# Kernel tuning notes

Hardware: AMD Instinct MI355X
Metric: run time of the kernel (lower is better)

The kernel has to match this reference:

```python
import math
import jax, jax.numpy as jnp
import numpy as np

# hyperparameters matching init_kwargs / spoco defaults
DELTA_VAR = 0.5
DELTA_DIST = 2.0
ALPHA = 1.0
BETA = 1.0
GAMMA = 0.001
INSTANCE_W = 1.0
PMAPS_THRESHOLD = 0.9  # gaussian-kernel threshold: pmap==PMAPS_THRESHOLD at dist==delta_var
EPS = 1e-6


def setup_inputs() -> dict:
    key = jax.random.key(0)
    k1, k2 = jax.random.split(key)
    N, E, H, W, C = 4, 64, 512, 512, 64
    embeddings = jax.random.normal(k1, (N, E, H, W), dtype=jnp.float32)
    target = jax.random.randint(k2, (N, H, W), 0, C)
    return {"embeddings": embeddings, "target": target, "n_instances": C}


def _single_item_loss(emb, tgt, C):
    """emb: (E,H,W) float, tgt: (H,W) int labels in [0,C). Returns scalar loss."""
    E = emb.shape[0]
    P = emb.shape[1] * emb.shape[2]
    e = emb.reshape(E, P)            # (E,P)
    t = tgt.reshape(P)               # (P,)

    # --- cluster means via segment reduce (math-equivalent to one-hot expand+sum) ---
    counts = jax.ops.segment_sum(jnp.ones((P,), e.dtype), t, num_segments=C)  # (C,)
    sums = jax.ops.segment_sum(e.T, t, num_segments=C)                         # (C,E)
    safe_counts = jnp.maximum(counts, 1.0)
    means = sums / safe_counts[:, None]                                        # (C,E)

    # --- variance (pull) term ---
    mean_at_pix = means[t]                                                     # (P,E)
    dist = jnp.sqrt(jnp.sum((e.T - mean_at_pix) ** 2, axis=1) + 1e-12)         # (P,)
    hinged = jnp.maximum(dist - DELTA_VAR, 0.0) ** 2                           # hinge_pull=True
    var_term = jnp.sum(hinged / safe_counts[t]) / C

    # --- distance (push) term between cluster means ---
    diff = means[:, None, :] - means[None, :, :]                               # (C,C,E)
    dmat = jnp.sqrt(jnp.sum(diff ** 2, axis=-1) + 1e-12)                       # (C,C)
    repulsion = 2.0 * DELTA_DIST * (1.0 - jnp.eye(C, dtype=e.dtype))
    hinged_d = jnp.maximum(repulsion - dmat, 0.0) ** 2
    dist_term = jnp.sum(hinged_d) / (C * (C - 1))

    # --- regularization term ---
    reg_term = jnp.sum(jnp.sqrt(jnp.sum(means ** 2, axis=1) + 1e-12)) / C

    # --- instance term: differentiable gaussian instance pmaps vs one-hot masks (dice) ---
    two_sigma = DELTA_VAR ** 2 / (-math.log(PMAPS_THRESHOLD))
    # squared distance of every pixel embedding to every cluster mean, (C,P)
    d2 = (jnp.sum(e ** 2, axis=0)[None, :]
          + jnp.sum(means ** 2, axis=1)[:, None]
          - 2.0 * means @ e)
    d2 = jnp.maximum(d2, 0.0)
    pmaps = jnp.exp(-d2 / two_sigma)                                           # (C,P)
    masks = (t[None, :] == jnp.arange(C)[:, None]).astype(e.dtype)             # (C,P)
    intersect = jnp.sum(pmaps * masks, axis=1)
    denom = jnp.sum(pmaps ** 2, axis=1) + jnp.sum(masks, axis=1)
    dice = 2.0 * intersect / jnp.maximum(denom, EPS)                            # (C,)
    instance_term = 1.0 - jnp.mean(dice)

    return (ALPHA * var_term + BETA * dist_term + GAMMA * reg_term
            + INSTANCE_W * instance_term)


def reference(embeddings, target, n_instances):
    per_item = jax.vmap(lambda e, t: _single_item_loss(e, t, n_instances))(embeddings, target)
    return jnp.mean(per_item)
```

## Files before the change

kernel.cpp:

```cpp
#include <hip/hip_runtime.h>
#include <math.h>

#define NIT 4
#define ED  64
#define CL  64
#define PX  262144

#define W_CNT 0
#define W_SUM 256
#define W_MSQ 16640
#define W_INT 16896
#define W_DEN 17152
#define W_VAR 17408
#define W_DR  17412
#define W_TOT 17416

__device__ __forceinline__ void atomAddG(float* p, float v){
  __hip_atomic_fetch_add(p, v, __ATOMIC_RELAXED, __HIP_MEMORY_SCOPE_AGENT);
}
__device__ __forceinline__ void atomAddL(float* p, float v){
  __hip_atomic_fetch_add(p, v, __ATOMIC_RELAXED, __HIP_MEMORY_SCOPE_WORKGROUP);
}

__global__ __launch_bounds__(256) void k_sums(const float* __restrict__ emb,
                                              const int* __restrict__ tgt,
                                              float* __restrict__ ws){
  __shared__ float s_sum[CL*65];
  __shared__ float s_cnt[CL];
  const int tid = threadIdx.x;
  for (int i = tid; i < CL*65; i += 256) s_sum[i] = 0.f;
  if (tid < CL) s_cnt[tid] = 0.f;
  __syncthreads();
  const int n   = blockIdx.x >> 7;
  const int blk = blockIdx.x & 127;
  const float* eb = emb + (size_t)n * ED * PX;
  const int*   tg = tgt + (size_t)n * PX;
  const int base = blk * 2048;
  const int4 t0 = *(const int4*)(tg + base + tid*4);
  const int4 t1 = *(const int4*)(tg + base + 1024 + tid*4);
  atomAddL(&s_cnt[t0.x], 1.f); atomAddL(&s_cnt[t0.y], 1.f);
  atomAddL(&s_cnt[t0.z], 1.f); atomAddL(&s_cnt[t0.w], 1.f);
  atomAddL(&s_cnt[t1.x], 1.f); atomAddL(&s_cnt[t1.y], 1.f);
  atomAddL(&s_cnt[t1.z], 1.f); atomAddL(&s_cnt[t1.w], 1.f);
  const int a0 = t0.x*65, a1 = t0.y*65, a2 = t0.z*65, a3 = t0.w*65;
  const int b0 = t1.x*65, b1 = t1.y*65, b2 = t1.z*65, b3 = t1.w*65;
  #pragma unroll 4
  for (int e = 0; e < ED; ++e){
    const float* row = eb + (size_t)e * PX + base;
    const float4 v0 = *(const float4*)(row + tid*4);
    const float4 v1 = *(const float4*)(row + 1024 + tid*4);
    atomAddL(&s_sum[a0+e], v0.x); atomAddL(&s_sum[a1+e], v0.y);
    atomAddL(&s_sum[a2+e], v0.z); atomAddL(&s_sum[a3+e], v0.w);
    atomAddL(&s_sum[b0+e], v1.x); atomAddL(&s_sum[b1+e], v1.y);
    atomAddL(&s_sum[b2+e], v1.z); atomAddL(&s_sum[b3+e], v1.w);
  }
  __syncthreads();
  float* wsum = ws + W_SUM + n*CL*ED;
  for (int i = tid; i < CL*ED; i += 256)
    atomAddG(&wsum[i], s_sum[(i>>6)*65 + (i&63)]);
  if (tid < CL) atomAddG(&ws[W_CNT + n*CL + tid], s_cnt[tid]);
}

__global__ __launch_bounds__(256) void k_fin(float* __restrict__ ws){
  __shared__ float sm[CL][ED+1];
  __shared__ float red[256];
  const int tid = threadIdx.x;
  const int n = blockIdx.x;
  float* wsum = ws + W_SUM + n*CL*ED;
  const float* wcnt = ws + W_CNT + n*CL;
  for (int i = tid; i < CL*ED; i += 256){
    const int c = i >> 6, e = i & 63;
    const float m = wsum[i] / fmaxf(wcnt[c], 1.f);
    sm[c][e] = m;
    wsum[i] = m;
  }
  __syncthreads();
  float reg_local = 0.f;
  if (tid < CL){
    float s = 0.f;
    #pragma unroll
    for (int e = 0; e < ED; ++e) s += sm[tid][e]*sm[tid][e];
    ws[W_MSQ + n*CL + tid] = s;
    reg_local = sqrtf(s + 1e-12f);
  }
  float pair_local = 0.f;
  for (int idx = tid; idx < CL*CL; idx += 256){
    const int i = idx >> 6, j = idx & 63;
    if (i != j){
      float s = 0.f;
      #pragma unroll
      for (int e = 0; e < ED; ++e){ const float d = sm[i][e]-sm[j][e]; s += d*d; }
      const float h = fmaxf(4.0f - sqrtf(s + 1e-12f), 0.f);
      pair_local += h*h;
    }
  }
  red[tid] = pair_local; __syncthreads();
  for (int s = 128; s > 0; s >>= 1){ if (tid < s) red[tid] += red[tid+s]; __syncthreads(); }
  const float pair_sum = red[0];
  __syncthreads();
  red[tid] = reg_local; __syncthreads();
  for (int s = 128; s > 0; s >>= 1){ if (tid < s) red[tid] += red[tid+s]; __syncthreads(); }
  if (tid == 0)
    ws[W_DR + n] = pair_sum / 4032.0f + 0.001f * red[0] / 64.0f;
}

__global__ __launch_bounds__(256) void k_main(const float* __restrict__ emb,
                                              const int* __restrict__ tgt,
                                              float* __restrict__ ws){
  __shared__ float s_m[CL*ED];
  __shared__ float s_msq[CL];
  __shared__ float s_icnt[CL];
  __shared__ float s_den[CL];
  __shared__ float s_int[CL];
  __shared__ float s_var[4];
  const int tid = threadIdx.x;
  const int n   = blockIdx.x >> 8;
  const int blk = blockIdx.x & 255;
  const float* wm = ws + W_SUM + n*CL*ED;
  for (int i = tid; i < CL*ED; i += 256) s_m[i] = wm[i];
  if (tid < CL){
    s_msq[tid] = ws[W_MSQ + n*CL + tid];
    s_icnt[tid] = 1.f / fmaxf(ws[W_CNT + n*CL + tid], 1.f);
    s_den[tid] = 0.f;
    s_int[tid] = 0.f;
  }
  __syncthreads();
  const float* eb = emb + (size_t)n * ED * PX;
  const int*   tg = tgt + (size_t)n * PX;
  const int lane = tid & 63;
  const float kExpScale = -0.42144206f;
  float var_local = 0.f;
  float den_mine = 0.f;
  for (int it = 0; it < 2; ++it){
    const int p0 = blk*1024 + it*512 + tid;
    const int p1 = p0 + 256;
    const int ta = tg[p0], tb = tg[p1];
    float ev0[ED], ev1[ED];
    float e2a = 0.f, e2b = 0.f;
    #pragma unroll
    for (int e = 0; e < ED; ++e){
      const float va = eb[(size_t)e*PX + p0];
      const float vb = eb[(size_t)e*PX + p1];
      ev0[e] = va; ev1[e] = vb;
      e2a += va*va; e2b += vb*vb;
    }
    float pmta = 0.f, pmtb = 0.f, d2ta = 0.f, d2tb = 0.f;
    #pragma unroll 2
    for (int c = 0; c < CL; ++c){
      const float4* mrow = (const float4*)&s_m[c*ED];
      float a0=0.f,a1=0.f,a2=0.f,a3=0.f, b0=0.f,b1=0.f,b2=0.f,b3=0.f;
      #pragma unroll
      for (int e4 = 0; e4 < ED/4; ++e4){
        const float4 m = mrow[e4];
        a0 += m.x*ev0[e4*4+0]; a1 += m.y*ev0[e4*4+1];
        a2 += m.z*ev0[e4*4+2]; a3 += m.w*ev0[e4*4+3];
        b0 += m.x*ev1[e4*4+0]; b1 += m.y*ev1[e4*4+1];
        b2 += m.z*ev1[e4*4+2]; b3 += m.w*ev1[e4*4+3];
      }
      const float dota = (a0+a1)+(a2+a3);
      const float dotb = (b0+b1)+(b2+b3);
      const float msq = s_msq[c];
      const float d2a = fmaxf(e2a + msq - 2.f*dota, 0.f);
      const float d2b = fmaxf(e2b + msq - 2.f*dotb, 0.f);
      const float pma = __expf(d2a * kExpScale);
      const float pmb = __expf(d2b * kExpScale);
      float r = pma*pma + pmb*pmb;
      #pragma unroll
      for (int m_ = 1; m_ < 64; m_ <<= 1) r += __shfl_xor(r, m_, 64);
      den_mine += (lane == c) ? r : 0.f;
      const bool oa = (c == ta), ob = (c == tb);
      pmta = oa ? pma : pmta; d2ta = oa ? d2a : d2ta;
      pmtb = ob ? pmb : pmtb; d2tb = ob ? d2b : d2tb;
    }
    atomAddL(&s_int[ta], pmta);
    atomAddL(&s_int[tb], pmtb);
    const float da = sqrtf(d2ta + 1e-12f), db = sqrtf(d2tb + 1e-12f);
    const float ha = fmaxf(da - 0.5f, 0.f), hb = fmaxf(db - 0.5f, 0.f);
    var_local += ha*ha*s_icnt[ta] + hb*hb*s_icnt[tb];
  }
  atomAddL(&s_den[lane], den_mine);
  #pragma unroll
  for (int m_ = 1; m_ < 64; m_ <<= 1) var_local += __shfl_xor(var_local, m_, 64);
  if (lane == 0) s_var[tid >> 6] = var_local;
  __syncthreads();
  if (tid < CL){
    atomAddG(&ws[W_DEN + n*CL + tid], s_den[tid]);
    atomAddG(&ws[W_INT + n*CL + tid], s_int[tid]);
  }
  if (tid == 0)
    atomAddG(&ws[W_VAR + n], s_var[0]+s_var[1]+s_var[2]+s_var[3]);
}

__global__ __launch_bounds__(256) void k_out(const float* __restrict__ ws,
                                             float* __restrict__ out){
  __shared__ float dsum[NIT];
  __shared__ float tot;
  const int tid = threadIdx.x;
  if (tid < NIT) dsum[tid] = 0.f;
  if (tid == 0) tot = 0.f;
  __syncthreads();
  const int n = tid >> 6, c = tid & 63;
  const float cnt   = ws[W_CNT + n*CL + c];
  const float inter = ws[W_INT + n*CL + c];
  const float den   = ws[W_DEN + n*CL + c] + cnt;
  const float dice  = 2.f * inter / fmaxf(den, 1e-6f);
  atomAddL(&dsum[n], dice);
  __syncthreads();
  if (tid < NIT){
    const float loss = ws[W_VAR + tid] / 64.0f
                     + ws[W_DR + tid]
                     + (1.f - dsum[tid] / 64.0f);
    atomAddL(&tot, loss);
  }
  __syncthreads();
  if (tid == 0) out[0] = tot * 0.25f;
}

extern "C" void kernel_launch(void* const* d_in, const int* in_sizes, int n_in,
                              void* d_out, int out_size, void* d_ws, size_t ws_size,
                              hipStream_t stream){
  (void)in_sizes; (void)n_in; (void)out_size; (void)ws_size;
  const float* emb = (const float*)d_in[0];
  const int*   tgt = (const int*)d_in[1];
  float* ws  = (float*)d_ws;
  float* out = (float*)d_out;
  hipMemsetAsync(d_ws, 0, W_TOT*sizeof(float), stream);
  k_sums<<<NIT*128, 256, 0, stream>>>(emb, tgt, ws);
  k_fin <<<NIT,     256, 0, stream>>>(ws);
  k_main<<<NIT*256, 256, 0, stream>>>(emb, tgt, ws);
  k_out <<<1,       256, 0, stream>>>(ws, out);
}
```

Baseline: 855.9 us.

## Remap sums and main kernels to lane-per-cluster with LDS-staged pixel tiles

Both the segment-sum and the main distance kernels now assign one cluster per lane and keep that cluster's mean or partial sum in registers. Each wave stages a tile of 32 pixels × 64 embedding dims into LDS and broadcasts each pixel to every lane. In the sums kernel this replaces per-element LDS atomics with masked FMAs. In the main kernel it replaces the per-cluster 64-lane shuffle reductions and the shared atomics with per-lane accumulators. The cost is heavy register pressure (64-float arrays) and redundant masked FMA work across all 64 lanes.

```diff
diff --git a/kernel.cpp b/kernel.cpp
--- a/kernel.cpp
+++ b/kernel.cpp
@@ -15,49 +15,87 @@
 #define W_DR  17412
 #define W_TOT 17416
 
+#define CHUNKS 8
+#define CPX 32
+#define RSTRIDE 68
+
 __device__ __forceinline__ void atomAddG(float* p, float v){
   __hip_atomic_fetch_add(p, v, __ATOMIC_RELAXED, __HIP_MEMORY_SCOPE_AGENT);
 }
-__device__ __forceinline__ void atomAddL(float* p, float v){
-  __hip_atomic_fetch_add(p, v, __ATOMIC_RELAXED, __HIP_MEMORY_SCOPE_WORKGROUP);
+__device__ __forceinline__ float readlanef(float v, int l){
+  return __uint_as_float(__builtin_amdgcn_readlane(__float_as_uint(v), l));
 }
 
 __global__ __launch_bounds__(256) void k_sums(const float* __restrict__ emb,
                                               const int* __restrict__ tgt,
                                               float* __restrict__ ws){
-  __shared__ float s_sum[CL*65];
+  __shared__ float s_px[4][CPX*RSTRIDE];
   __shared__ float s_cnt[CL];
-  const int tid = threadIdx.x;
-  for (int i = tid; i < CL*65; i += 256) s_sum[i] = 0.f;
-  if (tid < CL) s_cnt[tid] = 0.f;
-  __syncthreads();
-  const int n   = blockIdx.x >> 7;
-  const int blk = blockIdx.x & 127;
+  const int tid  = threadIdx.x;
+  const int lane = tid & 63;
+  const int w    = tid >> 6;
+  const int n    = blockIdx.x >> 8;
+  const int blk  = blockIdx.x & 255;
   const float* eb = emb + (size_t)n * ED * PX;
   const int*   tg = tgt + (size_t)n * PX;
-  const int base = blk * 2048;
-  const int4 t0 = *(const int4*)(tg + base + tid*4);
-  const int4 t1 = *(const int4*)(tg + base + 1024 + tid*4);
-  atomAddL(&s_cnt[t0.x], 1.f); atomAddL(&s_cnt[t0.y], 1.f);
-  atomAddL(&s_cnt[t0.z], 1.f); atomAddL(&s_cnt[t0.w], 1.f);
-  atomAddL(&s_cnt[t1.x], 1.f); atomAddL(&s_cnt[t1.y], 1.f);
-  atomAddL(&s_cnt[t1.z], 1.f); atomAddL(&s_cnt[t1.w], 1.f);
-  const int a0 = t0.x*65, a1 = t0.y*65, a2 = t0.z*65, a3 = t0.w*65;
-  const int b0 = t1.x*65, b1 = t1.y*65, b2 = t1.z*65, b3 = t1.w*65;
-  #pragma unroll 4
-  for (int e = 0; e < ED; ++e){
-    const float* row = eb + (size_t)e * PX + base;
-    const float4 v0 = *(const float4*)(row + tid*4);
-    const float4 v1 = *(const float4*)(row + 1024 + tid*4);
-    atomAddL(&s_sum[a0+e], v0.x); atomAddL(&s_sum[a1+e], v0.y);
-    atomAddL(&s_sum[a2+e], v0.z); atomAddL(&s_sum[a3+e], v0.w);
-    atomAddL(&s_sum[b0+e], v1.x); atomAddL(&s_sum[b1+e], v1.y);
-    atomAddL(&s_sum[b2+e], v1.z); atomAddL(&s_sum[b3+e], v1.w);
-  }
-  __syncthreads();
+  const int px4 = lane & 7;
+  const int eh  = lane >> 3;
+  float* srow = s_px[w];
+  float sum_r[ED];
+  #pragma unroll
+  for (int e = 0; e < ED; ++e) sum_r[e] = 0.f;
+  float cnt_r = 0.f;
+  const int wave_id = blk*4 + w;
+
+  for (int ch = 0; ch < CHUNKS; ++ch){
+    const int base = wave_id*(CHUNKS*CPX) + ch*CPX;
+    const int t_r = tg[base + (lane & 31)];
+    #pragma unroll
+    for (int e0 = 0; e0 < ED; e0 += 8){
+      const float4 v4 = *(const float4*)(eb + (size_t)(e0+eh)*PX + base + px4*4);
+      const int wb = px4*(4*RSTRIDE) + e0 + eh;
+      srow[wb]             = v4.x;
+      srow[wb +   RSTRIDE] = v4.y;
+      srow[wb + 2*RSTRIDE] = v4.z;
+      srow[wb + 3*RSTRIDE] = v4.w;
+    }
+    for (int j = 0; j < CPX; ++j){
+      const int tj = __builtin_amdgcn_readlane(t_r, j);
+      const float pf = (lane == tj) ? 1.f : 0.f;
+      cnt_r += pf;
+      const float4* row = (const float4*)(srow + j*RSTRIDE);
+      #pragma unroll
+      for (int k = 0; k < 16; ++k){
+        const float4 v = row[k];
+        sum_r[4*k+0] = fmaf(v.x, pf, sum_r[4*k+0]);
+        sum_r[4*k+1] = fmaf(v.y, pf, sum_r[4*k+1]);
+        sum_r[4*k+2] = fmaf(v.z, pf, sum_r[4*k+2]);
+        sum_r[4*k+3] = fmaf(v.w, pf, sum_r[4*k+3]);
+      }
+    }
+  }
+  float* s_acc = &s_px[0][0];
+  __syncthreads();
+  for (int w2 = 0; w2 < 4; ++w2){
+    if (w == w2){
+      if (w2 == 0){
+        #pragma unroll
+        for (int e = 0; e < ED; ++e) s_acc[lane*65+e] = sum_r[e];
+        if (w == 0) s_cnt[lane] = cnt_r;
+      } else {
+        #pragma unroll
+        for (int e = 0; e < ED; ++e) s_acc[lane*65+e] += sum_r[e];
+        s_cnt[lane] += cnt_r;
+      }
+    }
+    __syncthreads();
+  }
   float* wsum = ws + W_SUM + n*CL*ED;
-  for (int i = tid; i < CL*ED; i += 256)
-    atomAddG(&wsum[i], s_sum[(i>>6)*65 + (i&63)]);
+  #pragma unroll
+  for (int i = 0; i < 16; ++i){
+    const int idx = i*256 + tid;
+    atomAddG(&wsum[idx], s_acc[(idx>>6)*65 + (idx&63)]);
+  }
   if (tid < CL) atomAddG(&ws[W_CNT + n*CL + tid], s_cnt[tid]);
 }
 
@@ -107,88 +145,87 @@
 __global__ __launch_bounds__(256) void k_main(const float* __restrict__ emb,
                                               const int* __restrict__ tgt,
                                               float* __restrict__ ws){
-  __shared__ float s_m[CL*ED];
-  __shared__ float s_msq[CL];
-  __shared__ float s_icnt[CL];
-  __shared__ float s_den[CL];
-  __shared__ float s_int[CL];
-  __shared__ float s_var[4];
-  const int tid = threadIdx.x;
-  const int n   = blockIdx.x >> 8;
-  const int blk = blockIdx.x & 255;
-  const float* wm = ws + W_SUM + n*CL*ED;
-  for (int i = tid; i < CL*ED; i += 256) s_m[i] = wm[i];
-  if (tid < CL){
-    s_msq[tid] = ws[W_MSQ + n*CL + tid];
-    s_icnt[tid] = 1.f / fmaxf(ws[W_CNT + n*CL + tid], 1.f);
-    s_den[tid] = 0.f;
-    s_int[tid] = 0.f;
-  }
-  __syncthreads();
+  __shared__ float s_px[4][CPX*RSTRIDE];
+  const int tid  = threadIdx.x;
+  const int lane = tid & 63;
+  const int w    = tid >> 6;
+  const int n    = blockIdx.x >> 8;
+  const int blk  = blockIdx.x & 255;
   const float* eb = emb + (size_t)n * ED * PX;
   const int*   tg = tgt + (size_t)n * PX;
-  const int lane = tid & 63;
-  const float kExpScale = -0.42144206f;
-  float var_local = 0.f;
-  float den_mine = 0.f;
-  for (int it = 0; it < 2; ++it){
-    const int p0 = blk*1024 + it*512 + tid;
-    const int p1 = p0 + 256;
-    const int ta = tg[p0], tb = tg[p1];
-    float ev0[ED], ev1[ED];
-    float e2a = 0.f, e2b = 0.f;
-    #pragma unroll
-    for (int e = 0; e < ED; ++e){
-      const float va = eb[(size_t)e*PX + p0];
-      const float vb = eb[(size_t)e*PX + p1];
-      ev0[e] = va; ev1[e] = vb;
-      e2a += va*va; e2b += vb*vb;
-    }
-    float pmta = 0.f, pmtb = 0.f, d2ta = 0.f, d2tb = 0.f;
-    #pragma unroll 2
-    for (int c = 0; c < CL; ++c){
-      const float4* mrow = (const float4*)&s_m[c*ED];
-      float a0=0.f,a1=0.f,a2=0.f,a3=0.f, b0=0.f,b1=0.f,b2=0.f,b3=0.f;
+  const float* wm = ws + W_SUM + n*CL*ED;
+  float mean_r[ED];
+  #pragma unroll
+  for (int k = 0; k < 16; ++k){
+    const float4 m4 = *(const float4*)(wm + lane*ED + 4*k);
+    mean_r[4*k+0]=m4.x; mean_r[4*k+1]=m4.y; mean_r[4*k+2]=m4.z; mean_r[4*k+3]=m4.w;
+  }
+  const float msq  = ws[W_MSQ + n*CL + lane];
+  const float icnt = 1.f / fmaxf(ws[W_CNT + n*CL + lane], 1.f);
+  const int px4 = lane & 7;
+  const int eh  = lane >> 3;
+  float* srow = s_px[w];
+  float den_acc = 0.f, int_acc = 0.f, var_acc = 0.f;
+  const int wave_id = blk*4 + w;
+
+  for (int ch = 0; ch < CHUNKS; ++ch){
+    const int base = wave_id*(CHUNKS*CPX) + ch*CPX;
+    const int t_r = tg[base + (lane & 31)];
+    float e2p[4] = {0.f,0.f,0.f,0.f};
+    #pragma unroll
+    for (int e0 = 0; e0 < ED; e0 += 8){
+      const float4 v4 = *(const float4*)(eb + (size_t)(e0+eh)*PX + base + px4*4);
+      e2p[0] = fmaf(v4.x, v4.x, e2p[0]);
+      e2p[1] = fmaf(v4.y, v4.y, e2p[1]);
+      e2p[2] = fmaf(v4.z, v4.z, e2p[2]);
+      e2p[3] = fmaf(v4.w, v4.w, e2p[3]);
+      const int wb = px4*(4*RSTRIDE) + e0 + eh;
+      srow[wb]             = v4.x;
+      srow[wb +   RSTRIDE] = v4.y;
+      srow[wb + 2*RSTRIDE] = v4.z;
+      srow[wb + 3*RSTRIDE] = v4.w;
+    }
+    #pragma unroll
+    for (int m = 8; m < 64; m <<= 1){
+      e2p[0] += __shfl_xor(e2p[0], m, 64);
+      e2p[1] += __shfl_xor(e2p[1], m, 64);
+      e2p[2] += __shfl_xor(e2p[2], m, 64);
+      e2p[3] += __shfl_xor(e2p[3], m, 64);
+    }
+    for (int j4 = 0; j4 < CPX/4; ++j4){
       #pragma unroll
-      for (int e4 = 0; e4 < ED/4; ++e4){
-        const float4 m = mrow[e4];
-        a0 += m.x*ev0[e4*4+0]; a1 += m.y*ev0[e4*4+1];
-        a2 += m.z*ev0[e4*4+2]; a3 += m.w*ev0[e4*4+3];
-        b0 += m.x*ev1[e4*4+0]; b1 += m.y*ev1[e4*4+1];
-        b2 += m.z*ev1[e4*4+2]; b3 += m.w*ev1[e4*4+3];
+      for (int kk = 0; kk < 4; ++kk){
+        const int j = j4*4 + kk;
+        const float e2j = readlanef(e2p[kk], j4);
+        const int   tj  = __builtin_amdgcn_readlane(t_r, j);
+        float d0=0.f, d1=0.f, d2s=0.f, d3=0.f;
+        const float4* row = (const float4*)(srow + j*RSTRIDE);
+        #pragma unroll
+        for (int k = 0; k < 16; ++k){
+          const float4 v = row[k];
+          d0  = fmaf(mean_r[4*k+0], v.x, d0);
+          d1  = fmaf(mean_r[4*k+1], v.y, d1);
+          d2s = fmaf(mean_r[4*k+2], v.z, d2s);
+          d3  = fmaf(mean_r[4*k+3], v.w, d3);
+        }
+        const float dot = (d0+d1)+(d2s+d3);
+        const float dd  = fmaxf(e2j + msq - 2.f*dot, 0.f);
+        const float pm  = __expf(dd * -0.42144207f);
+        den_acc = fmaf(pm, pm, den_acc);
+        const bool own = (lane == tj);
+        int_acc += own ? pm : 0.f;
+        const float dist = sqrtf(dd + 1e-12f);
+        const float h = fmaxf(dist - 0.5f, 0.f);
+        var_acc += own ? h*h*icnt : 0.f;
       }
-      const float dota = (a0+a1)+(a2+a3);
-      const float dotb = (b0+b1)+(b2+b3);
-      const float msq = s_msq[c];
-      const float d2a = fmaxf(e2a + msq - 2.f*dota, 0.f);
-      const float d2b = fmaxf(e2b + msq - 2.f*dotb, 0.f);
-      const float pma = __expf(d2a * kExpScale);
-      const float pmb = __expf(d2b * kExpScale);
-      float r = pma*pma + pmb*pmb;
-      #pragma unroll
-      for (int m_ = 1; m_ < 64; m_ <<= 1) r += __shfl_xor(r, m_, 64);
-      den_mine += (lane == c) ? r : 0.f;
-      const bool oa = (c == ta), ob = (c == tb);
-      pmta = oa ? pma : pmta; d2ta = oa ? d2a : d2ta;
-      pmtb = ob ? pmb : pmtb; d2tb = ob ? d2b : d2tb;
-    }
-    atomAddL(&s_int[ta], pmta);
-    atomAddL(&s_int[tb], pmtb);
-    const float da = sqrtf(d2ta + 1e-12f), db = sqrtf(d2tb + 1e-12f);
-    const float ha = fmaxf(da - 0.5f, 0.f), hb = fmaxf(db - 0.5f, 0.f);
-    var_local += ha*ha*s_icnt[ta] + hb*hb*s_icnt[tb];
-  }
-  atomAddL(&s_den[lane], den_mine);
-  #pragma unroll
-  for (int m_ = 1; m_ < 64; m_ <<= 1) var_local += __shfl_xor(var_local, m_, 64);
-  if (lane == 0) s_var[tid >> 6] = var_local;
-  __syncthreads();
-  if (tid < CL){
-    atomAddG(&ws[W_DEN + n*CL + tid], s_den[tid]);
-    atomAddG(&ws[W_INT + n*CL + tid], s_int[tid]);
-  }
-  if (tid == 0)
-    atomAddG(&ws[W_VAR + n], s_var[0]+s_var[1]+s_var[2]+s_var[3]);
+    }
+  }
+  atomAddG(&ws[W_DEN + n*CL + lane], den_acc);
+  atomAddG(&ws[W_INT + n*CL + lane], int_acc);
+  #pragma unroll
+  for (int m = 1; m < 64; m <<= 1) var_acc += __shfl_xor(var_acc, m, 64);
+  if (lane == 0) atomAddG(&ws[W_VAR + n], var_acc);
+  (void)tid;
 }
 
 __global__ __launch_bounds__(256) void k_out(const float* __restrict__ ws,
@@ -204,13 +241,13 @@
   const float inter = ws[W_INT + n*CL + c];
   const float den   = ws[W_DEN + n*CL + c] + cnt;
   const float dice  = 2.f * inter / fmaxf(den, 1e-6f);
-  atomAddL(&dsum[n], dice);
+  __hip_atomic_fetch_add(&dsum[n], dice, __ATOMIC_RELAXED, __HIP_MEMORY_SCOPE_WORKGROUP);
   __syncthreads();
   if (tid < NIT){
     const float loss = ws[W_VAR + tid] / 64.0f
                      + ws[W_DR + tid]
                      + (1.f - dsum[tid] / 64.0f);
-    atomAddL(&tot, loss);
+    __hip_atomic_fetch_add(&tot, loss, __ATOMIC_RELAXED, __HIP_MEMORY_SCOPE_WORKGROUP);
   }
   __syncthreads();
   if (tid == 0) out[0] = tot * 0.25f;
@@ -225,7 +262,7 @@
   float* ws  = (float*)d_ws;
   float* out = (float*)d_out;
   hipMemsetAsync(d_ws, 0, W_TOT*sizeof(float), stream);
-  k_sums<<<NIT*128, 256, 0, stream>>>(emb, tgt, ws);
+  k_sums<<<NIT*256, 256, 0, stream>>>(emb, tgt, ws);
   k_fin <<<NIT,     256, 0, stream>>>(ws);
   k_main<<<NIT*256, 256, 0, stream>>>(emb, tgt, ws);
   k_out <<<1,       256, 0, stream>>>(ws, out);
```

Measured after the change: 701.0 us. 18.1% less time.
